# Kernel optimization log

Measured on AMD Instinct MI355X. Metric: run time of the kernel, lower is better.

## Reference

```python
import jax, jax.numpy as jnp
import numpy as np

# pywt Wavelet('db4') decomposition filters (8 taps)
DEC_LO = jnp.array([-0.010597401784997278, 0.032883011666982945, 0.030841381835986965,
                    -0.18703481171888114, -0.02798376941698385, 0.6308807679295904,
                    0.7148465705525415, 0.23037781330885523], dtype=jnp.float32)
DEC_HI = jnp.array([-0.23037781330885523, 0.7148465705525415, -0.6308807679295904,
                    -0.02798376941698385, 0.18703481171888114, 0.030841381835986965,
                    -0.032883011666982945, -0.010597401784997278], dtype=jnp.float32)
FLEN = 8
LEVEL = 3


def _dwt_last(x, f):
    """Single-level DWT along last axis, pywt 'symmetric' mode.
    out[i] = sum_k f[k] * ext[2i+1-k] (true convolution, downsample by 2)."""
    p = FLEN - 1
    pad = [(0, 0)] * (x.ndim - 1) + [(p, p)]
    xp = jnp.pad(x, pad, mode='symmetric')[..., 1:]
    n = x.shape[-1]
    out_len = (n + FLEN - 1) // 2
    f_rev = f[::-1]
    y = f_rev[0] * xp[..., 0:2 * out_len:2]
    for j in range(1, FLEN):  # fixed 8-tap loop
        y = y + f_rev[j] * xp[..., j:j + 2 * out_len:2]
    return y


def _dwt_h(x, f):
    # DWT along axis -2 (rows/H)
    return jnp.swapaxes(_dwt_last(jnp.swapaxes(x, -1, -2), f), -1, -2)


def _dwt2(x):
    # x: [B, H, W] -> (cA, cH, cV, cD), matching pywt dwt2 ('aa','da','ad','dd')
    lo_w = _dwt_last(x, DEC_LO)
    hi_w = _dwt_last(x, DEC_HI)
    cA = _dwt_h(lo_w, DEC_LO)  # low H,  low W
    cH = _dwt_h(lo_w, DEC_HI)  # high H, low W  (horizontal detail)
    cV = _dwt_h(hi_w, DEC_LO)  # low H,  high W (vertical detail)
    cD = _dwt_h(hi_w, DEC_HI)  # high H, high W (diagonal detail)
    return cA, cH, cV, cD


def setup_inputs() -> dict:
    key = jax.random.key(0)
    x = jax.random.normal(key, (16, 1, 1024, 1024), dtype=jnp.float32)
    return {"x": x}


def reference(x):
    # wavedec2 ordering: (cA_L, (cH_L, cV_L, cD_L), ..., (cH_1, cV_1, cD_1))
    a = x[:, 0]  # [B, H, W]
    details = []
    for _ in range(LEVEL):
        a, lh, hl, hh = _dwt2(a)
        details.insert(0, (lh, hl, hh))  # coarsest first, as pywt returns
    outs = [a[:, None]]  # [B,1,h,w]
    for lh, hl, hh in details:
        outs += [lh[:, None], hl[:, None], hh[:, None]]
    return tuple(outs)
```

## Files before the change

### kernel.cpp

```cpp
#include <hip/hip_runtime.h>

#define NT 256

__device__ __forceinline__ int refl(int i, int n) {
    i = (i < 0) ? (-i - 1) : i;
    i = (i >= n) ? (2 * n - 1 - i) : i;
    return i;
}

__global__ __launch_bounds__(256, 8)
void dwt2_fused(const float* __restrict__ in, int n, int ldin, int inb,
                int m, int nty, int ntx,
                float* __restrict__ oA, int ldA, int Ab,
                float* __restrict__ oH, float* __restrict__ oV, float* __restrict__ oD)
{
    constexpr float LOF[8] = {
        -0.010597401784997278f,  0.032883011666982945f,
         0.030841381835986965f, -0.18703481171888114f,
        -0.02798376941698385f,   0.6308807679295904f,
         0.7148465705525415f,    0.23037781330885523f };
    constexpr float HIF[8] = {
        -0.23037781330885523f,   0.7148465705525415f,
        -0.6308807679295904f,   -0.02798376941698385f,
         0.18703481171888114f,   0.030841381835986965f,
        -0.032883011666982945f, -0.010597401784997278f };

    __shared__ float s[70][66];

    const int nwg  = gridDim.x;
    const int wgid = blockIdx.x;
    const int q = nwg >> 3, r = nwg & 7;
    const int xcd = wgid & 7, pos = wgid >> 3;
    const int start = xcd * q + (xcd < r ? xcd : r);
    const int i = start + pos;
    const int ty = i % nty;
    const int t2 = i / nty;
    const int tx = t2 % ntx;
    const int b  = t2 / ntx;

    const int tid = threadIdx.x;
    const int c0 = tx * 32, r0 = ty * 32;
    const float* Ain = in + b * inb;

    const int rb = 2 * r0 - 6;
    const int cb = 2 * c0 - 8;

    const bool interior = (rb >= 0) && (rb + 69 < n) && (cb >= 0) && (cb + 71 < n);

    if (interior) {
        for (int idx = tid; idx < 560; idx += NT) {
            const int tr = idx >> 3, qc = idx & 7;
            const float* p = Ain + (rb + tr) * ldin + (cb + 8 * qc);
            const float4 a0 = *(const float4*)(p);
            const float4 a1 = *(const float4*)(p + 4);
            const float4 a2 = *(const float4*)(p + 8);
            const float4 a3 = *(const float4*)(p + 12);
            const float v[16] = { a0.x, a0.y, a0.z, a0.w,
                                  a1.x, a1.y, a1.z, a1.w,
                                  a2.x, a2.y, a2.z, a2.w,
                                  a3.x, a3.y, a3.z, a3.w };
            float* srow = &s[tr][8 * qc];
            #pragma unroll
            for (int d = 0; d < 4; ++d) {
                float lo = 0.f, hi = 0.f;
                #pragma unroll
                for (int k = 0; k < 8; ++k) {
                    const float x = v[2 * d + 9 - k];
                    lo += LOF[k] * x;
                    hi += HIF[k] * x;
                }
                *(float2*)(srow + 2 * d) = make_float2(lo, hi);
            }
        }
    } else {
        for (int idx = tid; idx < 560; idx += NT) {
            const int tr = idx >> 3, qc = idx & 7;
            const float* row = Ain + refl(rb + tr, n) * ldin;
            const int cw = cb + 8 * qc;
            float v[16];
            v[0] = 0.f; v[1] = 0.f;
            #pragma unroll
            for (int u = 2; u < 16; ++u) v[u] = row[refl(cw + u, n)];
            float* srow = &s[tr][8 * qc];
            #pragma unroll
            for (int d = 0; d < 4; ++d) {
                float lo = 0.f, hi = 0.f;
                #pragma unroll
                for (int k = 0; k < 8; ++k) {
                    const float x = v[2 * d + 9 - k];
                    lo += LOF[k] * x;
                    hi += HIF[k] * x;
                }
                *(float2*)(srow + 2 * d) = make_float2(lo, hi);
            }
        }
    }
    __syncthreads();

    const int ob = b * (m * m);
    const int oa = b * Ab;
    for (int idx = tid; idx < 512; idx += NT) {
        const int c = idx & 31, pr = idx >> 5;
        float lo[10], hi[10];
        #pragma unroll
        for (int j = 0; j < 10; ++j) {
            const float2 w = *(const float2*)&s[4 * pr + j][2 * c];
            lo[j] = w.x; hi[j] = w.y;
        }
        float A0 = 0.f, H0 = 0.f, V0 = 0.f, D0 = 0.f;
        float A1 = 0.f, H1 = 0.f, V1 = 0.f, D1 = 0.f;
        #pragma unroll
        for (int k = 0; k < 8; ++k) {
            const float l0 = lo[7 - k], h0 = hi[7 - k];
            const float l1 = lo[9 - k], h1 = hi[9 - k];
            A0 += LOF[k] * l0;  H0 += HIF[k] * l0;
            V0 += LOF[k] * h0;  D0 += HIF[k] * h0;
            A1 += LOF[k] * l1;  H1 += HIF[k] * l1;
            V1 += LOF[k] * h1;  D1 += HIF[k] * h1;
        }
        const int gr = r0 + 2 * pr, gc = c0 + c;
        if (gc < m) {
            const int od = gr * m + gc;
            if (gr < m) {
                oA[oa + gr * ldA + gc] = A0;
                oH[ob + od] = H0; oV[ob + od] = V0; oD[ob + od] = D0;
            }
            if (gr + 1 < m) {
                oA[oa + (gr + 1) * ldA + gc] = A1;
                oH[ob + od + m] = H1; oV[ob + od + m] = V1; oD[ob + od + m] = D1;
            }
        }
    }
}

extern "C" void kernel_launch(void* const* d_in, const int* in_sizes, int n_in,
                              void* d_out, int out_size, void* d_ws, size_t ws_size,
                              hipStream_t stream) {
    const float* x = (const float*)d_in[0];
    float* out = (float*)d_out;
    float* ws  = (float*)d_ws;

    const int B = 16;
    const int n1 = 1024, m1 = 515;
    const int n2 = 515,  m2 = 261;
    const int n3 = 261,  m3 = 134;

    const int ld1 = 516, b1 = m1 * ld1;
    const int ld2 = 264, b2 = m2 * ld2;
    float* a1 = ws;
    float* a2 = ws + (size_t)b1 * B;

    const size_t sz1 = (size_t)B * m1 * m1;
    const size_t sz2 = (size_t)B * m2 * m2;
    const size_t sz3 = (size_t)B * m3 * m3;

    float* a3  = out;
    float* lh3 = a3  + sz3;
    float* hl3 = lh3 + sz3;
    float* hh3 = hl3 + sz3;
    float* lh2 = hh3 + sz3;
    float* hl2 = lh2 + sz2;
    float* hh2 = hl2 + sz2;
    float* lh1 = hh2 + sz2;
    float* hl1 = lh1 + sz1;
    float* hh1 = hl1 + sz1;

    const int t1 = (m1 + 31) / 32;
    const int t2_ = (m2 + 31) / 32;
    const int t3 = (m3 + 31) / 32;

    dim3 blk(NT);
    dim3 g1(t1 * t1 * B, 1, 1);
    dim3 g2(t2_ * t2_ * B, 1, 1);
    dim3 g3(t3 * t3 * B, 1, 1);

    dwt2_fused<<<g1, blk, 0, stream>>>(x,  n1, n1, n1 * n1,
                                       m1, t1, t1, a1, ld1, b1, lh1, hl1, hh1);
    dwt2_fused<<<g2, blk, 0, stream>>>(a1, n2, ld1, b1,
                                       m2, t2_, t2_, a2, ld2, b2, lh2, hl2, hh2);
    dwt2_fused<<<g3, blk, 0, stream>>>(a2, n3, ld2, b2,
                                       m3, t3, t3, out, m3, m3 * m3, lh3, hl3, hh3);
}
```

Measured before the change: 58.87 us.

## Make DWT kernel persistent with register prefetch of next tile's input

Measured after the change: 64.53 us. 1.1x slower.

```diff
diff --git a/kernel.cpp b/kernel.cpp
--- a/kernel.cpp
+++ b/kernel.cpp
@@ -1,6 +1,6 @@
 #include <hip/hip_runtime.h>
 
-#define NT 256
+#define NT 320
 
 __device__ __forceinline__ int refl(int i, int n) {
     i = (i < 0) ? (-i - 1) : i;
@@ -8,11 +8,12 @@
     return i;
 }
 
-__global__ __launch_bounds__(256, 8)
+__global__ __launch_bounds__(NT)
 void dwt2_fused(const float* __restrict__ in, int n, int ldin, int inb,
-                int m, int nty, int ntx,
+                int m, int nty, int ntx, int ntiles,
                 float* __restrict__ oA, int ldA, int Ab,
-                float* __restrict__ oH, float* __restrict__ oV, float* __restrict__ oD)
+                float* __restrict__ oH, float* __restrict__ oV,
+                float* __restrict__ oD)
 {
     constexpr float LOF[8] = {
         -0.010597401784997278f,  0.032883011666982945f,
@@ -27,109 +28,125 @@
 
     __shared__ float s[70][66];
 
-    const int nwg  = gridDim.x;
-    const int wgid = blockIdx.x;
-    const int q = nwg >> 3, r = nwg & 7;
-    const int xcd = wgid & 7, pos = wgid >> 3;
-    const int start = xcd * q + (xcd < r ? xcd : r);
-    const int i = start + pos;
-    const int ty = i % nty;
-    const int t2 = i / nty;
-    const int tx = t2 % ntx;
-    const int b  = t2 / ntx;
-
     const int tid = threadIdx.x;
-    const int c0 = tx * 32, r0 = ty * 32;
-    const float* Ain = in + b * inb;
-
-    const int rb = 2 * r0 - 6;
-    const int cb = 2 * c0 - 8;
-
-    const bool interior = (rb >= 0) && (rb + 69 < n) && (cb >= 0) && (cb + 71 < n);
-
-    if (interior) {
-        for (int idx = tid; idx < 560; idx += NT) {
-            const int tr = idx >> 3, qc = idx & 7;
-            const float* p = Ain + (rb + tr) * ldin + (cb + 8 * qc);
-            const float4 a0 = *(const float4*)(p);
-            const float4 a1 = *(const float4*)(p + 4);
-            const float4 a2 = *(const float4*)(p + 8);
-            const float4 a3 = *(const float4*)(p + 12);
-            const float v[16] = { a0.x, a0.y, a0.z, a0.w,
-                                  a1.x, a1.y, a1.z, a1.w,
-                                  a2.x, a2.y, a2.z, a2.w,
-                                  a3.x, a3.y, a3.z, a3.w };
-            float* srow = &s[tr][8 * qc];
+    const int G = gridDim.x;
+
+    const int q = G >> 3, r = G & 7;
+    const int xcd = blockIdx.x & 7, pos = blockIdx.x >> 3;
+    const int gp = xcd * q + (xcd < r ? xcd : r) + pos;
+
+    const int t_lo = (gp * ntiles) / G;
+    const int t_hi = ((gp + 1) * ntiles) / G;
+
+    const bool hasA = (tid < 280);
+    const int a_tr = tid >> 2, a_oc8 = tid & 3;
+
+    float va[24];
+
+    {
+        const int t = t_lo;
+        if (hasA) {
+            const int ty = t % nty; const int u2 = t / nty;
+            const int tx = u2 % ntx; const int b = u2 / ntx;
+            const float* Ain = in + b * inb;
+            const int rr = 2 * (ty * 32) - 6 + a_tr;
+            const int cw = 2 * (tx * 32) - 8 + 16 * a_oc8;
+            if (rr >= 0 && rr < n && cw >= 0 && cw + 23 < n) {
+                const float* p = Ain + rr * ldin + cw;
+                #pragma unroll
+                for (int j = 0; j < 6; ++j) {
+                    const float4 t4 = *(const float4*)(p + 4 * j);
+                    va[4*j] = t4.x; va[4*j+1] = t4.y; va[4*j+2] = t4.z; va[4*j+3] = t4.w;
+                }
+            } else {
+                const float* row = Ain + refl(rr, n) * ldin;
+                #pragma unroll
+                for (int u = 0; u < 24; ++u) va[u] = row[refl(cw + u, n)];
+            }
+        }
+    }
+
+    for (int t = t_lo; t < t_hi; ++t) {
+        const int ty = t % nty; const int u2 = t / nty;
+        const int tx = u2 % ntx; const int b = u2 / ntx;
+        const int c0 = tx * 32, r0 = ty * 32;
+
+        if (hasA) {
+            float* srow = &s[a_tr][16 * a_oc8];
             #pragma unroll
-            for (int d = 0; d < 4; ++d) {
+            for (int d = 0; d < 8; ++d) {
                 float lo = 0.f, hi = 0.f;
                 #pragma unroll
                 for (int k = 0; k < 8; ++k) {
-                    const float x = v[2 * d + 9 - k];
+                    const float x = va[2 * d + 9 - k];
                     lo += LOF[k] * x;
                     hi += HIF[k] * x;
                 }
                 *(float2*)(srow + 2 * d) = make_float2(lo, hi);
             }
         }
-    } else {
-        for (int idx = tid; idx < 560; idx += NT) {
-            const int tr = idx >> 3, qc = idx & 7;
-            const float* row = Ain + refl(rb + tr, n) * ldin;
-            const int cw = cb + 8 * qc;
-            float v[16];
-            v[0] = 0.f; v[1] = 0.f;
-            #pragma unroll
-            for (int u = 2; u < 16; ++u) v[u] = row[refl(cw + u, n)];
-            float* srow = &s[tr][8 * qc];
-            #pragma unroll
-            for (int d = 0; d < 4; ++d) {
-                float lo = 0.f, hi = 0.f;
+        __syncthreads();
+
+        if (t + 1 < t_hi && hasA) {
+            const int nt_ = t + 1;
+            const int ty2 = nt_ % nty; const int u3 = nt_ / nty;
+            const int tx2 = u3 % ntx; const int b2 = u3 / ntx;
+            const float* Ain = in + b2 * inb;
+            const int rr = 2 * (ty2 * 32) - 6 + a_tr;
+            const int cw = 2 * (tx2 * 32) - 8 + 16 * a_oc8;
+            if (rr >= 0 && rr < n && cw >= 0 && cw + 23 < n) {
+                const float* p = Ain + rr * ldin + cw;
+                #pragma unroll
+                for (int j = 0; j < 6; ++j) {
+                    const float4 t4 = *(const float4*)(p + 4 * j);
+                    va[4*j] = t4.x; va[4*j+1] = t4.y; va[4*j+2] = t4.z; va[4*j+3] = t4.w;
+                }
+            } else {
+                const float* row = Ain + refl(rr, n) * ldin;
+                #pragma unroll
+                for (int u = 0; u < 24; ++u) va[u] = row[refl(cw + u, n)];
+            }
+        }
+
+        const int ob = b * (m * m);
+        const int oa = b * Ab;
+        #pragma unroll
+        for (int half = 0; half < 2; ++half) {
+            const int idx = tid + half * NT;
+            if (idx < 512) {
+                const int c = idx & 31, pr = idx >> 5;
+                float lov[10], hiv[10];
+                #pragma unroll
+                for (int j = 0; j < 10; ++j) {
+                    const float2 w = *(const float2*)&s[4 * pr + j][2 * c];
+                    lov[j] = w.x; hiv[j] = w.y;
+                }
+                float A0 = 0.f, H0 = 0.f, V0 = 0.f, D0 = 0.f;
+                float A1 = 0.f, H1 = 0.f, V1 = 0.f, D1 = 0.f;
                 #pragma unroll
                 for (int k = 0; k < 8; ++k) {
-                    const float x = v[2 * d + 9 - k];
-                    lo += LOF[k] * x;
-                    hi += HIF[k] * x;
-                }
-                *(float2*)(srow + 2 * d) = make_float2(lo, hi);
-            }
-        }
-    }
-    __syncthreads();
-
-    const int ob = b * (m * m);
-    const int oa = b * Ab;
-    for (int idx = tid; idx < 512; idx += NT) {
-        const int c = idx & 31, pr = idx >> 5;
-        float lo[10], hi[10];
-        #pragma unroll
-        for (int j = 0; j < 10; ++j) {
-            const float2 w = *(const float2*)&s[4 * pr + j][2 * c];
-            lo[j] = w.x; hi[j] = w.y;
-        }
-        float A0 = 0.f, H0 = 0.f, V0 = 0.f, D0 = 0.f;
-        float A1 = 0.f, H1 = 0.f, V1 = 0.f, D1 = 0.f;
-        #pragma unroll
-        for (int k = 0; k < 8; ++k) {
-            const float l0 = lo[7 - k], h0 = hi[7 - k];
-            const float l1 = lo[9 - k], h1 = hi[9 - k];
-            A0 += LOF[k] * l0;  H0 += HIF[k] * l0;
-            V0 += LOF[k] * h0;  D0 += HIF[k] * h0;
-            A1 += LOF[k] * l1;  H1 += HIF[k] * l1;
-            V1 += LOF[k] * h1;  D1 += HIF[k] * h1;
-        }
-        const int gr = r0 + 2 * pr, gc = c0 + c;
-        if (gc < m) {
-            const int od = gr * m + gc;
-            if (gr < m) {
-                oA[oa + gr * ldA + gc] = A0;
-                oH[ob + od] = H0; oV[ob + od] = V0; oD[ob + od] = D0;
-            }
-            if (gr + 1 < m) {
-                oA[oa + (gr + 1) * ldA + gc] = A1;
-                oH[ob + od + m] = H1; oV[ob + od + m] = V1; oD[ob + od + m] = D1;
-            }
-        }
+                    const float l0 = lov[7 - k], h0 = hiv[7 - k];
+                    const float l1 = lov[9 - k], h1 = hiv[9 - k];
+                    A0 += LOF[k] * l0;  H0 += HIF[k] * l0;
+                    V0 += LOF[k] * h0;  D0 += HIF[k] * h0;
+                    A1 += LOF[k] * l1;  H1 += HIF[k] * l1;
+                    V1 += LOF[k] * h1;  D1 += HIF[k] * h1;
+                }
+                const int gr = r0 + 2 * pr, gc = c0 + c;
+                if (gc < m) {
+                    const int od = gr * m + gc;
+                    if (gr < m) {
+                        oA[oa + gr * ldA + gc] = A0;
+                        oH[ob + od] = H0; oV[ob + od] = V0; oD[ob + od] = D0;
+                    }
+                    if (gr + 1 < m) {
+                        oA[oa + (gr + 1) * ldA + gc] = A1;
+                        oH[ob + od + m] = H1; oV[ob + od + m] = V1; oD[ob + od + m] = D1;
+                    }
+                }
+            }
+        }
+        __syncthreads();
     }
 }
 
@@ -169,15 +186,22 @@
     const int t2_ = (m2 + 31) / 32;
     const int t3 = (m3 + 31) / 32;
 
+    const int nt1 = t1 * t1 * B;
+    const int nt2 = t2_ * t2_ * B;
+    const int nt3 = t3 * t3 * B;
+
+    const int G1 = 1536;
+    const int G2 = (nt2 < 1536) ? nt2 : 1536;
+    const int G3 = (nt3 < 1536) ? nt3 : 1536;
+
     dim3 blk(NT);
-    dim3 g1(t1 * t1 * B, 1, 1);
-    dim3 g2(t2_ * t2_ * B, 1, 1);
-    dim3 g3(t3 * t3 * B, 1, 1);
-
-    dwt2_fused<<<g1, blk, 0, stream>>>(x,  n1, n1, n1 * n1,
-                                       m1, t1, t1, a1, ld1, b1, lh1, hl1, hh1);
-    dwt2_fused<<<g2, blk, 0, stream>>>(a1, n2, ld1, b1,
-                                       m2, t2_, t2_, a2, ld2, b2, lh2, hl2, hh2);
-    dwt2_fused<<<g3, blk, 0, stream>>>(a2, n3, ld2, b2,
-                                       m3, t3, t3, out, m3, m3 * m3, lh3, hl3, hh3);
+    dwt2_fused<<<dim3(G1), blk, 0, stream>>>(x,  n1, n1, n1 * n1,
+                                             m1, t1, t1, nt1,
+                                             a1, ld1, b1, lh1, hl1, hh1);
+    dwt2_fused<<<dim3(G2), blk, 0, stream>>>(a1, n2, ld1, b1,
+                                             m2, t2_, t2_, nt2,
+                                             a2, ld2, b2, lh2, hl2, hh2);
+    dwt2_fused<<<dim3(G3), blk, 0, stream>>>(a2, n3, ld2, b2,
+                                             m3, t3, t3, nt3,
+                                             out, m3, m3 * m3, lh3, hl3, hh3);
 }
```

## Store row-filtered intermediates as packed bf16 in LDS and use 512-thread blocks

Applied to the files above, without the earlier changes.

Result: no change. 58.35 us (-0.9%).

```diff
diff --git a/kernel.cpp b/kernel.cpp
--- a/kernel.cpp
+++ b/kernel.cpp
@@ -1,6 +1,6 @@
 #include <hip/hip_runtime.h>
 
-#define NT 256
+#define NT 512
 
 __device__ __forceinline__ int refl(int i, int n) {
     i = (i < 0) ? (-i - 1) : i;
@@ -8,11 +8,26 @@
     return i;
 }
 
-__global__ __launch_bounds__(256, 8)
+__device__ __forceinline__ unsigned bpack(float lo, float hi) {
+    union { float f; unsigned u; } a, b;
+    a.f = lo; b.f = hi;
+    const unsigned ua = (a.u + 0x7FFFu + ((a.u >> 16) & 1u)) >> 16;
+    const unsigned ub = (b.u + 0x7FFFu + ((b.u >> 16) & 1u)) & 0xFFFF0000u;
+    return ua | ub;
+}
+__device__ __forceinline__ float b_lo(unsigned u) {
+    union { unsigned u; float f; } x; x.u = u << 16; return x.f;
+}
+__device__ __forceinline__ float b_hi(unsigned u) {
+    union { unsigned u; float f; } x; x.u = u & 0xFFFF0000u; return x.f;
+}
+
+__global__ __launch_bounds__(NT, 8)
 void dwt2_fused(const float* __restrict__ in, int n, int ldin, int inb,
                 int m, int nty, int ntx,
                 float* __restrict__ oA, int ldA, int Ab,
-                float* __restrict__ oH, float* __restrict__ oV, float* __restrict__ oD)
+                float* __restrict__ oH, float* __restrict__ oV,
+                float* __restrict__ oD)
 {
     constexpr float LOF[8] = {
         -0.010597401784997278f,  0.032883011666982945f,
@@ -25,14 +40,12 @@
          0.18703481171888114f,   0.030841381835986965f,
         -0.032883011666982945f, -0.010597401784997278f };
 
-    __shared__ float s[70][66];
-
-    const int nwg  = gridDim.x;
-    const int wgid = blockIdx.x;
-    const int q = nwg >> 3, r = nwg & 7;
-    const int xcd = wgid & 7, pos = wgid >> 3;
-    const int start = xcd * q + (xcd < r ? xcd : r);
-    const int i = start + pos;
+    __shared__ unsigned s[70 * 36];
+
+    const int G = gridDim.x;
+    const int q = G >> 3, rm = G & 7;
+    const int xcd = blockIdx.x & 7, pos = blockIdx.x >> 3;
+    const int i = xcd * q + (xcd < rm ? xcd : rm) + pos;
     const int ty = i % nty;
     const int t2 = i / nty;
     const int tx = t2 % ntx;
@@ -42,93 +55,111 @@
     const int c0 = tx * 32, r0 = ty * 32;
     const float* Ain = in + b * inb;
 
-    const int rb = 2 * r0 - 6;
-    const int cb = 2 * c0 - 8;
-
-    const bool interior = (rb >= 0) && (rb + 69 < n) && (cb >= 0) && (cb + 71 < n);
-
+    const int rb  = 2 * r0 - 6;
+    const int cw0 = 2 * c0 - 8;
+
+    const bool interior = (rb >= 0) && (rb + 69 < n) && (cw0 >= 0) && (cw0 + 71 < n);
+
+    const int tr0 = tid >> 3, g0 = tid & 7;
+    const bool has2 = (tid < 48);
+    const int tr1 = 64 + (tid >> 3), g1 = tid & 7;
+
+    float v0[16], v1[16];
     if (interior) {
-        for (int idx = tid; idx < 560; idx += NT) {
-            const int tr = idx >> 3, qc = idx & 7;
-            const float* p = Ain + (rb + tr) * ldin + (cb + 8 * qc);
-            const float4 a0 = *(const float4*)(p);
-            const float4 a1 = *(const float4*)(p + 4);
-            const float4 a2 = *(const float4*)(p + 8);
-            const float4 a3 = *(const float4*)(p + 12);
-            const float v[16] = { a0.x, a0.y, a0.z, a0.w,
-                                  a1.x, a1.y, a1.z, a1.w,
-                                  a2.x, a2.y, a2.z, a2.w,
-                                  a3.x, a3.y, a3.z, a3.w };
-            float* srow = &s[tr][8 * qc];
+        const float* p0 = Ain + (rb + tr0) * ldin + (cw0 + 8 * g0);
+        const float4 a0 = ((const float4*)p0)[0];
+        const float4 a1 = ((const float4*)p0)[1];
+        const float4 a2 = ((const float4*)p0)[2];
+        const float4 a3 = ((const float4*)p0)[3];
+        v0[0]=a0.x; v0[1]=a0.y; v0[2]=a0.z; v0[3]=a0.w;
+        v0[4]=a1.x; v0[5]=a1.y; v0[6]=a1.z; v0[7]=a1.w;
+        v0[8]=a2.x; v0[9]=a2.y; v0[10]=a2.z; v0[11]=a2.w;
+        v0[12]=a3.x; v0[13]=a3.y; v0[14]=a3.z; v0[15]=a3.w;
+        if (has2) {
+            const float* p1 = Ain + (rb + tr1) * ldin + (cw0 + 8 * g1);
+            const float4 b0 = ((const float4*)p1)[0];
+            const float4 b1 = ((const float4*)p1)[1];
+            const float4 b2 = ((const float4*)p1)[2];
+            const float4 b3 = ((const float4*)p1)[3];
+            v1[0]=b0.x; v1[1]=b0.y; v1[2]=b0.z; v1[3]=b0.w;
+            v1[4]=b1.x; v1[5]=b1.y; v1[6]=b1.z; v1[7]=b1.w;
+            v1[8]=b2.x; v1[9]=b2.y; v1[10]=b2.z; v1[11]=b2.w;
+            v1[12]=b3.x; v1[13]=b3.y; v1[14]=b3.z; v1[15]=b3.w;
+        }
+    } else {
+        const float* row0 = Ain + refl(rb + tr0, n) * ldin;
+        const int cb0 = cw0 + 8 * g0;
+        #pragma unroll
+        for (int u = 0; u < 16; ++u) v0[u] = row0[refl(cb0 + u, n)];
+        if (has2) {
+            const float* row1 = Ain + refl(rb + tr1, n) * ldin;
+            const int cb1 = cw0 + 8 * g1;
             #pragma unroll
-            for (int d = 0; d < 4; ++d) {
-                float lo = 0.f, hi = 0.f;
-                #pragma unroll
-                for (int k = 0; k < 8; ++k) {
-                    const float x = v[2 * d + 9 - k];
-                    lo += LOF[k] * x;
-                    hi += HIF[k] * x;
-                }
-                *(float2*)(srow + 2 * d) = make_float2(lo, hi);
+            for (int u = 0; u < 16; ++u) v1[u] = row1[refl(cb1 + u, n)];
+        }
+    }
+
+    {
+        unsigned w[4];
+        #pragma unroll
+        for (int d = 0; d < 4; ++d) {
+            float lo = 0.f, hi = 0.f;
+            #pragma unroll
+            for (int k = 0; k < 8; ++k) {
+                const float x = v0[2 * d + 9 - k];
+                lo += LOF[k] * x;
+                hi += HIF[k] * x;
             }
-        }
-    } else {
-        for (int idx = tid; idx < 560; idx += NT) {
-            const int tr = idx >> 3, qc = idx & 7;
-            const float* row = Ain + refl(rb + tr, n) * ldin;
-            const int cw = cb + 8 * qc;
-            float v[16];
-            v[0] = 0.f; v[1] = 0.f;
+            w[d] = bpack(lo, hi);
+        }
+        *(uint4*)&s[tr0 * 36 + 4 * g0] = make_uint4(w[0], w[1], w[2], w[3]);
+    }
+    if (has2) {
+        unsigned w[4];
+        #pragma unroll
+        for (int d = 0; d < 4; ++d) {
+            float lo = 0.f, hi = 0.f;
             #pragma unroll
-            for (int u = 2; u < 16; ++u) v[u] = row[refl(cw + u, n)];
-            float* srow = &s[tr][8 * qc];
-            #pragma unroll
-            for (int d = 0; d < 4; ++d) {
-                float lo = 0.f, hi = 0.f;
-                #pragma unroll
-                for (int k = 0; k < 8; ++k) {
-                    const float x = v[2 * d + 9 - k];
-                    lo += LOF[k] * x;
-                    hi += HIF[k] * x;
-                }
-                *(float2*)(srow + 2 * d) = make_float2(lo, hi);
+            for (int k = 0; k < 8; ++k) {
+                const float x = v1[2 * d + 9 - k];
+                lo += LOF[k] * x;
+                hi += HIF[k] * x;
             }
-        }
+            w[d] = bpack(lo, hi);
+        }
+        *(uint4*)&s[tr1 * 36 + 4 * g1] = make_uint4(w[0], w[1], w[2], w[3]);
     }
     __syncthreads();
 
-    const int ob = b * (m * m);
-    const int oa = b * Ab;
-    for (int idx = tid; idx < 512; idx += NT) {
-        const int c = idx & 31, pr = idx >> 5;
-        float lo[10], hi[10];
-        #pragma unroll
-        for (int j = 0; j < 10; ++j) {
-            const float2 w = *(const float2*)&s[4 * pr + j][2 * c];
-            lo[j] = w.x; hi[j] = w.y;
-        }
-        float A0 = 0.f, H0 = 0.f, V0 = 0.f, D0 = 0.f;
-        float A1 = 0.f, H1 = 0.f, V1 = 0.f, D1 = 0.f;
-        #pragma unroll
-        for (int k = 0; k < 8; ++k) {
-            const float l0 = lo[7 - k], h0 = hi[7 - k];
-            const float l1 = lo[9 - k], h1 = hi[9 - k];
-            A0 += LOF[k] * l0;  H0 += HIF[k] * l0;
-            V0 += LOF[k] * h0;  D0 += HIF[k] * h0;
-            A1 += LOF[k] * l1;  H1 += HIF[k] * l1;
-            V1 += LOF[k] * h1;  D1 += HIF[k] * h1;
-        }
-        const int gr = r0 + 2 * pr, gc = c0 + c;
-        if (gc < m) {
-            const int od = gr * m + gc;
-            if (gr < m) {
-                oA[oa + gr * ldA + gc] = A0;
-                oH[ob + od] = H0; oV[ob + od] = V0; oD[ob + od] = D0;
-            }
-            if (gr + 1 < m) {
-                oA[oa + (gr + 1) * ldA + gc] = A1;
-                oH[ob + od + m] = H1; oV[ob + od + m] = V1; oD[ob + od + m] = D1;
-            }
+    const int c = tid & 31, pr = tid >> 5;
+    float lov[10], hiv[10];
+    #pragma unroll
+    for (int j = 0; j < 10; ++j) {
+        const unsigned u = s[(4 * pr + j) * 36 + c];
+        lov[j] = b_lo(u); hiv[j] = b_hi(u);
+    }
+    float A0 = 0.f, H0 = 0.f, V0 = 0.f, D0 = 0.f;
+    float A1 = 0.f, H1 = 0.f, V1 = 0.f, D1 = 0.f;
+    #pragma unroll
+    for (int k = 0; k < 8; ++k) {
+        const float l0 = lov[7 - k], h0 = hiv[7 - k];
+        const float l1 = lov[9 - k], h1 = hiv[9 - k];
+        A0 += LOF[k] * l0;  H0 += HIF[k] * l0;
+        V0 += LOF[k] * h0;  D0 += HIF[k] * h0;
+        A1 += LOF[k] * l1;  H1 += HIF[k] * l1;
+        V1 += LOF[k] * h1;  D1 += HIF[k] * h1;
+    }
+    const int gr = r0 + 2 * pr, gc = c0 + c;
+    if (gc < m) {
+        const int ob = b * (m * m);
+        const int od = ob + gr * m + gc;
+        if (gr < m) {
+            oA[b * Ab + gr * ldA + gc] = A0;
+            oH[od] = H0; oV[od] = V0; oD[od] = D0;
+        }
+        if (gr + 1 < m) {
+            oA[b * Ab + (gr + 1) * ldA + gc] = A1;
+            oH[od + m] = H1; oV[od + m] = V1; oD[od + m] = D1;
         }
     }
 }
```
